# Performance work log

Hardware: AMD Instinct MI355X
Metric: run time of the kernel (lower is better)

The kernel has to match this reference:

```python
import jax, jax.numpy as jnp
import numpy as np

N = 50000      # nodes
DEG = 16       # in-degree per node -> E = 800k edges
IN = 256       # in_size
HID = 32       # hid_size
HEAD = 4       # heads in first layer
OUT = 40       # out_size (classes)
HH = HID * HEAD  # 128, hidden width
NEG_SLOPE = 0.2


def setup_inputs() -> dict:
    key = jax.random.key(0)
    ks = jax.random.split(key, 16)
    E = N * DEG
    src = jax.random.randint(ks[0], (E,), 0, N)
    dst = jnp.repeat(jnp.arange(N), DEG)  # every node has DEG in-edges

    def nrm(k, shape):
        return jax.random.normal(k, shape, jnp.float32) * 0.1

    return dict(
        features=jax.random.normal(ks[1], (N, IN), jnp.float32),
        src=src, dst=dst,
        # layer 1: GATConv(IN -> HID, HEAD heads)
        W1=nrm(ks[2], (IN, HH)), al1=nrm(ks[3], (HEAD, HID)), ar1=nrm(ks[4], (HEAD, HID)), b1=nrm(ks[5], (HH,)),
        # hidden layer: GATConv(HH -> HH, 1 head)
        Wh=nrm(ks[6], (HH, HH)), alh=nrm(ks[7], (1, HH)), arh=nrm(ks[8], (1, HH)), bh=nrm(ks[9], (HH,)),
        # layer 2: GATConv(HH -> OUT, 1 head)
        W2=nrm(ks[10], (HH, OUT)), al2=nrm(ks[11], (1, OUT)), ar2=nrm(ks[12], (1, OUT)), b2=nrm(ks[13], (OUT,)),
    )


def gat_conv(x, src, dst, W, al, ar, b):
    """DGL-style GATConv. x:[N,F], W:[F,H*D], al/ar:[H,D], b:[H*D]. Returns [N,H,D]."""
    n = x.shape[0]
    H, D = al.shape
    feat = (x @ W).reshape(n, H, D)                 # [N,H,D]
    el = jnp.sum(feat * al, axis=-1)                # [N,H]
    er = jnp.sum(feat * ar, axis=-1)                # [N,H]
    e = jax.nn.leaky_relu(el[src] + er[dst], NEG_SLOPE)  # [E,H] per-edge logits
    # segment softmax over each destination's in-edges
    emax = jax.lax.stop_gradient(jax.ops.segment_max(e, dst, num_segments=n))  # [N,H]
    ex = jnp.exp(e - emax[dst])                     # [E,H]
    den = jax.ops.segment_sum(ex, dst, num_segments=n)  # [N,H]
    alpha = ex / den[dst]                           # [E,H]
    out = jax.ops.segment_sum(feat[src] * alpha[:, :, None], dst, num_segments=n)  # [N,H,D]
    return out + b.reshape(1, H, D)


def reference(features, src, dst, W1, al1, ar1, b1, Wh, alh, arh, bh, W2, al2, ar2, b2):
    # conv1 -> flatten heads -> relu
    h = jax.nn.relu(gat_conv(features, src, dst, W1, al1, ar1, b1).reshape(N, HH))
    # hidden GATConv (1 head) -> mean over head -> relu (dropout is identity in eval)
    h = jax.nn.relu(gat_conv(h, src, dst, Wh, alh, arh, bh).mean(axis=1))
    # conv2 (1 head) -> mean over head -> log_softmax
    h = gat_conv(h, src, dst, W2, al2, ar2, b2).mean(axis=1)
    return jax.nn.log_softmax(h, axis=1)
```

## Files before the change

kernel.cpp:

```cpp
#include <hip/hip_runtime.h>
#include <cstddef>
#include <math.h>

#define NN 50000
#define DEG 16
#define NEG_SLOPE 0.2f

typedef __attribute__((ext_vector_type(8))) short bf16x8;
typedef __attribute__((ext_vector_type(4))) float f32x4;

__device__ inline unsigned short f2bf(float x) {
    unsigned u = __float_as_uint(x);
    return (unsigned short)((u + 0x7FFF + ((u >> 16) & 1)) >> 16);
}
__device__ inline float bf2f(unsigned short u) {
    return __uint_as_float(((unsigned)u) << 16);
}
__device__ inline unsigned pack_bf2(float lo, float hi) {
    return (unsigned)f2bf(lo) | ((unsigned)f2bf(hi) << 16);
}
__device__ inline void gld_lds16(const unsigned short* g, unsigned short* l) {
    __builtin_amdgcn_global_load_lds((const __attribute__((address_space(1))) void*)g,
                                     (__attribute__((address_space(3))) void*)l, 16, 0, 0);
}

__global__ void prep_k(const float* __restrict__ W1, unsigned short* __restrict__ Wt1,
                       const float* __restrict__ Wh, unsigned short* __restrict__ Wth,
                       const float* __restrict__ feats, unsigned short* __restrict__ fb)
{
    const int b = blockIdx.x;
    if (b < 128) {
        int idx = b * 256 + threadIdx.x;
        int c = idx >> 8, k = idx & 255;
        Wt1[idx] = f2bf(W1[(size_t)k * 128 + c]);
    } else if (b < 192) {
        int idx = (b - 128) * 256 + threadIdx.x;
        int c = idx >> 7, k = idx & 127;
        Wth[idx] = f2bf(Wh[(size_t)k * 128 + c]);
    } else {
        int i = (b - 192) * 256 + threadIdx.x;
        const float4* p = (const float4*)feats + (size_t)i * 2;
        float4 v0 = p[0], v1 = p[1];
        uint4 o;
        o.x = pack_bf2(v0.x, v0.y);
        o.y = pack_bf2(v0.z, v0.w);
        o.z = pack_bf2(v1.x, v1.y);
        o.w = pack_bf2(v1.z, v1.w);
        *(uint4*)&fb[(size_t)i * 8] = o;
    }
}

__launch_bounds__(256)
__global__ void gemm1_k(const unsigned short* __restrict__ A,
                        const unsigned short* __restrict__ Wt,
                        const float* __restrict__ al, const float* __restrict__ ar,
                        unsigned short* __restrict__ feat,
                        float* __restrict__ el, float* __restrict__ er)
{
    constexpr int K = 256, KS = K / 32, SLOTS = K * 2, PARTS = SLOTS / 256, TPB = 4;
    __shared__ __align__(16) unsigned short buf[2][SLOTS * 8];
    const int tid = threadIdx.x;
    const int w = tid >> 6, l = tid & 63;
    const int lr = l & 15, lq = l >> 4;
    const int col0 = w * 32;

    bf16x8 B0[KS], B1[KS];
#pragma unroll
    for (int ks = 0; ks < KS; ks++) {
        B0[ks] = *(const bf16x8*)(Wt + (size_t)(col0 + lr) * K + ks * 32 + lq * 8);
        B1[ks] = *(const bf16x8*)(Wt + (size_t)(col0 + 16 + lr) * K + ks * 32 + lq * 8);
    }

    const int t0 = blockIdx.x * TPB;
    const int tmax = NN / 16;
    const int t1 = (t0 + TPB < tmax) ? t0 + TPB : tmax;
    if (t0 >= tmax) return;

    auto stage = [&](int t, int b) {
#pragma unroll
        for (int p = 0; p < PARTS; p++) {
            int j = tid + p * 256;
            int row = t * 16 + (j & 15);
            int koff = (j >> 6) * 32 + ((j >> 4) & 3) * 8;
            gld_lds16(A + (size_t)row * K + koff, &buf[b][(size_t)j * 8]);
        }
    };
    stage(t0, t0 & 1);

    for (int t = t0; t < t1; ++t) {
        __syncthreads();
        if (t + 1 < t1) stage(t + 1, (t + 1) & 1);

        f32x4 acc0 = {0.f, 0.f, 0.f, 0.f}, acc1 = {0.f, 0.f, 0.f, 0.f};
        const unsigned short* bb = buf[t & 1];
#pragma unroll
        for (int ks = 0; ks < KS; ks++) {
            bf16x8 a = *(const bf16x8*)(bb + (size_t)(ks * 64 + l) * 8);
            acc0 = __builtin_amdgcn_mfma_f32_16x16x32_bf16(a, B0[ks], acc0, 0, 0, 0);
            acc1 = __builtin_amdgcn_mfma_f32_16x16x32_bf16(a, B1[ks], acc1, 0, 0, 0);
        }

        const int row0 = t * 16;
#pragma unroll
        for (int reg = 0; reg < 4; reg++) {
            const int r = row0 + lq * 4 + reg;
            feat[(size_t)r * 128 + col0 + lr]      = f2bf(acc0[reg]);
            feat[(size_t)r * 128 + col0 + 16 + lr] = f2bf(acc1[reg]);
        }

        float pe[4], pr[4];
#pragma unroll
        for (int reg = 0; reg < 4; reg++) {
            pe[reg] = acc0[reg] * al[col0 + lr] + acc1[reg] * al[col0 + 16 + lr];
            pr[reg] = acc0[reg] * ar[col0 + lr] + acc1[reg] * ar[col0 + 16 + lr];
        }
#pragma unroll
        for (int m = 1; m < 16; m <<= 1)
#pragma unroll
            for (int reg = 0; reg < 4; reg++) {
                pe[reg] += __shfl_xor(pe[reg], m);
                pr[reg] += __shfl_xor(pr[reg], m);
            }
        if (lr == 0) {
#pragma unroll
            for (int reg = 0; reg < 4; reg++) {
                const int r = row0 + lq * 4 + reg;
                el[r * 4 + w] = pe[reg];
                er[r * 4 + w] = pr[reg];
            }
        }
    }
}

__launch_bounds__(256)
__global__ void fusedh_k(const unsigned short* __restrict__ feat1,
                         const float* __restrict__ el1, const float* __restrict__ er1,
                         const int* __restrict__ src, const float* __restrict__ b1,
                         const unsigned short* __restrict__ Wt,
                         const float* __restrict__ alh, const float* __restrict__ arh,
                         unsigned short* __restrict__ feat2,
                         float* __restrict__ el, float* __restrict__ er)
{
    __shared__ __align__(16) unsigned short abuf[256 * 8];
    __shared__ float s_alpha[16][64];
    __shared__ float redE[4][16], redR[4][16];
    const int tid = threadIdx.x;
    const int w = tid >> 6, lane = tid & 63;
    const int q = lane >> 4, li = lane & 15;
    const int slot = w * 4 + q;
    const int row0 = blockIdx.x * 16;
    const int node = row0 + slot;
    const int col0 = w * 32;

    bf16x8 B0[4], B1[4];
#pragma unroll
    for (int ks = 0; ks < 4; ks++) {
        B0[ks] = *(const bf16x8*)(Wt + (size_t)(col0 + li) * 128 + ks * 32 + q * 8);
        B1[ks] = *(const bf16x8*)(Wt + (size_t)(col0 + 16 + li) * 128 + ks * 32 + q * 8);
    }

    const int s = src[node * DEG + li];
    {
        const float4 elv = *(const float4*)(el1 + (size_t)s * 4);
        const float4 erv = *(const float4*)(er1 + (size_t)node * 4);
        float e[4] = {elv.x + erv.x, elv.y + erv.y, elv.z + erv.z, elv.w + erv.w};
#pragma unroll
        for (int h = 0; h < 4; h++) {
            float x = e[h];
            x = (x > 0.f) ? x : NEG_SLOPE * x;
            float mx = x;
#pragma unroll
            for (int d = 1; d < 16; d <<= 1) mx = fmaxf(mx, __shfl_xor(mx, d, 16));
            float ex = expf(x - mx);
            float den = ex;
#pragma unroll
            for (int d = 1; d < 16; d <<= 1) den += __shfl_xor(den, d, 16);
            s_alpha[slot][h * 16 + li] = ex / den;
        }
    }
    uint4 v[16];
#pragma unroll
    for (int jj = 0; jj < 16; jj++) {
        int sj = __shfl(s, (lane & 48) | jj);
        v[jj] = *(const uint4*)(feat1 + (size_t)sj * 128 + li * 8);
    }
    float acc[8] = {0.f, 0.f, 0.f, 0.f, 0.f, 0.f, 0.f, 0.f};
    const int hrow = (li >> 2) * 16;
#pragma unroll
    for (int jj = 0; jj < 16; jj++) {
        float a = s_alpha[slot][hrow + jj];
        unsigned u0 = v[jj].x, u1 = v[jj].y, u2 = v[jj].z, u3 = v[jj].w;
        acc[0] += a * bf2f((unsigned short)(u0 & 0xFFFF));
        acc[1] += a * bf2f((unsigned short)(u0 >> 16));
        acc[2] += a * bf2f((unsigned short)(u1 & 0xFFFF));
        acc[3] += a * bf2f((unsigned short)(u1 >> 16));
        acc[4] += a * bf2f((unsigned short)(u2 & 0xFFFF));
        acc[5] += a * bf2f((unsigned short)(u2 >> 16));
        acc[6] += a * bf2f((unsigned short)(u3 & 0xFFFF));
        acc[7] += a * bf2f((unsigned short)(u3 >> 16));
    }
    const float4 bb0 = *(const float4*)(b1 + li * 8);
    const float4 bb1 = *(const float4*)(b1 + li * 8 + 4);
    float o[8];
    o[0] = fmaxf(acc[0] + bb0.x, 0.f); o[1] = fmaxf(acc[1] + bb0.y, 0.f);
    o[2] = fmaxf(acc[2] + bb0.z, 0.f); o[3] = fmaxf(acc[3] + bb0.w, 0.f);
    o[4] = fmaxf(acc[4] + bb1.x, 0.f); o[5] = fmaxf(acc[5] + bb1.y, 0.f);
    o[6] = fmaxf(acc[6] + bb1.z, 0.f); o[7] = fmaxf(acc[7] + bb1.w, 0.f);
    {
        uint4 pk;
        pk.x = pack_bf2(o[0], o[1]);
        pk.y = pack_bf2(o[2], o[3]);
        pk.z = pack_bf2(o[4], o[5]);
        pk.w = pack_bf2(o[6], o[7]);
        int jw = ((li >> 2) * 64 + (li & 3) * 16 + slot) ^ (li & 7);
        *(uint4*)&abuf[(size_t)jw * 8] = pk;
    }
    __syncthreads();

    f32x4 acc0 = {0.f, 0.f, 0.f, 0.f}, acc1 = {0.f, 0.f, 0.f, 0.f};
#pragma unroll
    for (int ks = 0; ks < 4; ks++) {
        int jr = (ks * 64 + lane) ^ ((ks * 4 + q) & 7);
        bf16x8 a = *(const bf16x8*)&abuf[(size_t)jr * 8];
        acc0 = __builtin_amdgcn_mfma_f32_16x16x32_bf16(a, B0[ks], acc0, 0, 0, 0);
        acc1 = __builtin_amdgcn_mfma_f32_16x16x32_bf16(a, B1[ks], acc1, 0, 0, 0);
    }

#pragma unroll
    for (int reg = 0; reg < 4; reg++) {
        const int r = row0 + q * 4 + reg;
        feat2[(size_t)r * 128 + col0 + li]      = f2bf(acc0[reg]);
        feat2[(size_t)r * 128 + col0 + 16 + li] = f2bf(acc1[reg]);
    }
    float pe[4], pr[4];
#pragma unroll
    for (int reg = 0; reg < 4; reg++) {
        pe[reg] = acc0[reg] * alh[col0 + li] + acc1[reg] * alh[col0 + 16 + li];
        pr[reg] = acc0[reg] * arh[col0 + li] + acc1[reg] * arh[col0 + 16 + li];
    }
#pragma unroll
    for (int m = 1; m < 16; m <<= 1)
#pragma unroll
        for (int reg = 0; reg < 4; reg++) {
            pe[reg] += __shfl_xor(pe[reg], m);
            pr[reg] += __shfl_xor(pr[reg], m);
        }
    if (li == 0) {
#pragma unroll
        for (int reg = 0; reg < 4; reg++) {
            redE[w][q * 4 + reg] = pe[reg];
            redR[w][q * 4 + reg] = pr[reg];
        }
    }
    __syncthreads();
    if (tid < 16) {
        el[row0 + tid] = redE[0][tid] + redE[1][tid] + redE[2][tid] + redE[3][tid];
        er[row0 + tid] = redR[0][tid] + redR[1][tid] + redR[2][tid] + redR[3][tid];
    }
}

__launch_bounds__(256)
__global__ void fused40_k(const unsigned short* __restrict__ feat2,
                          const float* __restrict__ elA, const float* __restrict__ erA,
                          const int* __restrict__ src, const float* __restrict__ bh,
                          const float* __restrict__ W2,
                          const float* __restrict__ al2, const float* __restrict__ ar2,
                          unsigned short* __restrict__ f40,
                          float* __restrict__ el2, float* __restrict__ er2)
{
    __shared__ float As[32][132];
    __shared__ float Ws[128 * 40];
    const int tid = threadIdx.x;
    const int w = tid >> 6, lane = tid & 63;
    const int q = lane >> 4, li = lane & 15;
    const int slot = w * 4 + q;
    const int row0 = blockIdx.x * 32;

    {
        const float4* s4 = (const float4*)W2;
        float4* d4 = (float4*)Ws;
#pragma unroll
        for (int p = 0; p < 5; p++) d4[tid + 256 * p] = s4[tid + 256 * p];
    }

#pragma unroll
    for (int rnd = 0; rnd < 2; rnd++) {
        const int row = rnd * 16 + slot;
        int node = row0 + row;
        if (node > NN - 1) node = NN - 1;
        const int s = src[node * DEG + li];
        float x = elA[s] + erA[node];
        x = (x > 0.f) ? x : NEG_SLOPE * x;
        float mx = x;
#pragma unroll
        for (int d = 1; d < 16; d <<= 1) mx = fmaxf(mx, __shfl_xor(mx, d, 16));
        float ex = expf(x - mx);
        float den = ex;
#pragma unroll
        for (int d = 1; d < 16; d <<= 1) den += __shfl_xor(den, d, 16);
        const float alpha = ex / den;

        uint4 v[16];
#pragma unroll
        for (int jj = 0; jj < 16; jj++) {
            int sj = __shfl(s, (lane & 48) | jj);
            v[jj] = *(const uint4*)(feat2 + (size_t)sj * 128 + li * 8);
        }
        float acc[8] = {0.f, 0.f, 0.f, 0.f, 0.f, 0.f, 0.f, 0.f};
#pragma unroll
        for (int jj = 0; jj < 16; jj++) {
            float a = __shfl(alpha, (lane & 48) | jj);
            unsigned u0 = v[jj].x, u1 = v[jj].y, u2 = v[jj].z, u3 = v[jj].w;
            acc[0] += a * bf2f((unsigned short)(u0 & 0xFFFF));
            acc[1] += a * bf2f((unsigned short)(u0 >> 16));
            acc[2] += a * bf2f((unsigned short)(u1 & 0xFFFF));
            acc[3] += a * bf2f((unsigned short)(u1 >> 16));
            acc[4] += a * bf2f((unsigned short)(u2 & 0xFFFF));
            acc[5] += a * bf2f((unsigned short)(u2 >> 16));
            acc[6] += a * bf2f((unsigned short)(u3 & 0xFFFF));
            acc[7] += a * bf2f((unsigned short)(u3 >> 16));
        }
        const float4 bb0 = *(const float4*)(bh + li * 8);
        const float4 bb1 = *(const float4*)(bh + li * 8 + 4);
        float4 o0, o1;
        o0.x = fmaxf(acc[0] + bb0.x, 0.f); o0.y = fmaxf(acc[1] + bb0.y, 0.f);
        o0.z = fmaxf(acc[2] + bb0.z, 0.f); o0.w = fmaxf(acc[3] + bb0.w, 0.f);
        o1.x = fmaxf(acc[4] + bb1.x, 0.f); o1.y = fmaxf(acc[5] + bb1.y, 0.f);
        o1.z = fmaxf(acc[6] + bb1.z, 0.f); o1.w = fmaxf(acc[7] + bb1.w, 0.f);
        *(float4*)&As[row][li * 8]     = o0;
        *(float4*)&As[row][li * 8 + 4] = o1;
    }
    __syncthreads();

    const int tx = tid & 31;
    const int ty = tid >> 5;
    const int ctx = (tx < 20) ? tx : 19;
    const float2* Wf2 = (const float2*)Ws;
    float acc[4][2] = {};
#pragma unroll 4
    for (int k = 0; k < 128; k++) {
        float2 wv = Wf2[k * 20 + ctx];
#pragma unroll
        for (int i = 0; i < 4; i++) {
            float a = As[ty * 4 + i][k];
            acc[i][0] += a * wv.x;
            acc[i][1] += a * wv.y;
        }
    }
    float pel[4], per[4];
#pragma unroll
    for (int i = 0; i < 4; i++) {
        float vl = 0.f, vr = 0.f;
        if (tx < 20) {
            vl = acc[i][0] * al2[2 * ctx] + acc[i][1] * al2[2 * ctx + 1];
            vr = acc[i][0] * ar2[2 * ctx] + acc[i][1] * ar2[2 * ctx + 1];
        }
        pel[i] = vl; per[i] = vr;
    }
#pragma unroll
    for (int m = 1; m < 32; m <<= 1) {
#pragma unroll
        for (int i = 0; i < 4; i++) {
            pel[i] += __shfl_xor(pel[i], m);
            per[i] += __shfl_xor(per[i], m);
        }
    }
#pragma unroll
    for (int i = 0; i < 4; i++) {
        int r = row0 + ty * 4 + i;
        if (r < NN) {
            if (tx < 20) *(unsigned*)&f40[(size_t)r * 40 + 2 * tx] = pack_bf2(acc[i][0], acc[i][1]);
            if (tx == 0) { el2[r] = pel[i]; er2[r] = per[i]; }
        }
    }
}

__launch_bounds__(256)
__global__ void agg40_ls_k(const unsigned short* __restrict__ feat, const float* __restrict__ el,
                           const float* __restrict__ er, const int* __restrict__ src,
                           const float* __restrict__ bias, float* __restrict__ out)
{
    __shared__ float s_alpha[8][DEG];
    __shared__ int s_src[8][DEG];
    const int tid = threadIdx.x;
    const int w = tid >> 6, lane = tid & 63;
    const int half = lane >> 5, li = lane & 31;
    const int slot = w * 2 + half;
    const int node = blockIdx.x * 8 + slot;
    const int j = li & 15;

    int s = src[node * DEG + j];
    float e = el[s] + er[node];
    e = (e > 0.f) ? e : NEG_SLOPE * e;
    float mx = e;
#pragma unroll
    for (int d = 1; d < 16; d <<= 1) mx = fmaxf(mx, __shfl_xor(mx, d));
    float ex = expf(e - mx);
    float den = ex;
#pragma unroll
    for (int d = 1; d < 16; d <<= 1) den += __shfl_xor(den, d);
    if (li < 16) { s_alpha[slot][j] = ex / den; s_src[slot][j] = s; }
    __syncthreads();

    float acc0 = 0.f, acc1 = 0.f;
    if (li < 20) {
#pragma unroll
        for (int jj = 0; jj < DEG; jj++) {
            int sj = s_src[slot][jj];
            float a = s_alpha[slot][jj];
            unsigned v = *(const unsigned*)(feat + (size_t)sj * 40 + 2 * li);
            acc0 += a * bf2f((unsigned short)(v & 0xFFFF));
            acc1 += a * bf2f((unsigned short)(v >> 16));
        }
    }
    float v0 = acc0 + bias[2 * li], v1 = acc1 + bias[2 * li + 1];
    float m2 = (li < 20) ? fmaxf(v0, v1) : -INFINITY;
#pragma unroll
    for (int d = 1; d < 32; d <<= 1) m2 = fmaxf(m2, __shfl_xor(m2, d));
    float pe = (li < 20) ? (expf(v0 - m2) + expf(v1 - m2)) : 0.f;
    float se = pe;
#pragma unroll
    for (int d = 1; d < 32; d <<= 1) se += __shfl_xor(se, d);
    if (li < 20) {
        float ls = m2 + logf(se);
        out[(size_t)node * 40 + 2 * li]     = v0 - ls;
        out[(size_t)node * 40 + 2 * li + 1] = v1 - ls;
    }
}

extern "C" void kernel_launch(void* const* d_in, const int* in_sizes, int n_in,
                              void* d_out, int out_size, void* d_ws, size_t ws_size,
                              hipStream_t stream)
{
    const float* features = (const float*)d_in[0];
    const int*   src      = (const int*)d_in[1];
    const float* W1  = (const float*)d_in[3];
    const float* al1 = (const float*)d_in[4];
    const float* ar1 = (const float*)d_in[5];
    const float* b1  = (const float*)d_in[6];
    const float* Wh  = (const float*)d_in[7];
    const float* alh = (const float*)d_in[8];
    const float* arh = (const float*)d_in[9];
    const float* bh  = (const float*)d_in[10];
    const float* W2  = (const float*)d_in[11];
    const float* al2 = (const float*)d_in[12];
    const float* ar2 = (const float*)d_in[13];
    const float* b2  = (const float*)d_in[14];
    float* out = (float*)d_out;

    float* ws = (float*)d_ws;
    unsigned short* featb  = (unsigned short*)ws;
    unsigned short* featb2 = featb + (size_t)NN * 128;
    float* el1  = (float*)(featb2 + (size_t)NN * 128);
    float* er1  = el1 + (size_t)NN * 4;
    float* elA  = er1 + (size_t)NN * 4;
    float* erA  = elA + NN;
    float* el2  = erA + NN;
    float* er2  = el2 + NN;
    unsigned short* f40b = (unsigned short*)(er2 + NN);
    unsigned short* Wt1  = f40b + (size_t)NN * 40;
    unsigned short* Wth  = Wt1 + 128 * 256;
    unsigned short* featbf = Wth + 128 * 128;

    dim3 blk(256);
    prep_k<<<6442, blk, 0, stream>>>(W1, Wt1, Wh, Wth, features, featbf);
    gemm1_k<<<782, blk, 0, stream>>>(featbf, Wt1, al1, ar1, featb, el1, er1);
    fusedh_k<<<3125, blk, 0, stream>>>(featb, el1, er1, src, b1, Wth, alh, arh,
                                       featb2, elA, erA);
    fused40_k<<<1563, blk, 0, stream>>>(featb2, elA, erA, src, bh, W2, al2, ar2,
                                        f40b, el2, er2);
    agg40_ls_k<<<6250, blk, 0, stream>>>(f40b, el2, er2, src, b2, out);
}
```

Before: 121.7 us.

## Fuse fp32-to-bf16 feature conversion into gemm1 and drop LDS staging in aggregation

The separate pass that converted the 50000x256 fp32 feature matrix to bf16 is removed. gemm1 now stages fp32 rows into LDS with an XOR swizzle and converts to bf16 just before the MFMA, which saves a full write and re-read of the converted features. Weight loads in fusedh and the W2 copy in fused40 are moved later, after the gather/softmax phase, to shorten register live ranges and overlap. agg40 replaces its shared-memory alpha/src staging and block barrier with warp shuffles. The trade-off is twice the LDS traffic and footprint in gemm1 plus per-element conversion ALU work inside the MFMA loop.

```diff
diff --git a/kernel.cpp b/kernel.cpp
--- a/kernel.cpp
+++ b/kernel.cpp
@@ -19,46 +19,35 @@
 __device__ inline unsigned pack_bf2(float lo, float hi) {
     return (unsigned)f2bf(lo) | ((unsigned)f2bf(hi) << 16);
 }
-__device__ inline void gld_lds16(const unsigned short* g, unsigned short* l) {
+__device__ inline void gld_lds16f(const float* g, float* l) {
     __builtin_amdgcn_global_load_lds((const __attribute__((address_space(1))) void*)g,
                                      (__attribute__((address_space(3))) void*)l, 16, 0, 0);
 }
 
 __global__ void prep_k(const float* __restrict__ W1, unsigned short* __restrict__ Wt1,
-                       const float* __restrict__ Wh, unsigned short* __restrict__ Wth,
-                       const float* __restrict__ feats, unsigned short* __restrict__ fb)
+                       const float* __restrict__ Wh, unsigned short* __restrict__ Wth)
 {
     const int b = blockIdx.x;
     if (b < 128) {
         int idx = b * 256 + threadIdx.x;
         int c = idx >> 8, k = idx & 255;
         Wt1[idx] = f2bf(W1[(size_t)k * 128 + c]);
-    } else if (b < 192) {
+    } else {
         int idx = (b - 128) * 256 + threadIdx.x;
         int c = idx >> 7, k = idx & 127;
         Wth[idx] = f2bf(Wh[(size_t)k * 128 + c]);
-    } else {
-        int i = (b - 192) * 256 + threadIdx.x;
-        const float4* p = (const float4*)feats + (size_t)i * 2;
-        float4 v0 = p[0], v1 = p[1];
-        uint4 o;
-        o.x = pack_bf2(v0.x, v0.y);
-        o.y = pack_bf2(v0.z, v0.w);
-        o.z = pack_bf2(v1.x, v1.y);
-        o.w = pack_bf2(v1.z, v1.w);
-        *(uint4*)&fb[(size_t)i * 8] = o;
     }
 }
 
 __launch_bounds__(256)
-__global__ void gemm1_k(const unsigned short* __restrict__ A,
+__global__ void gemm1_k(const float* __restrict__ A,
                         const unsigned short* __restrict__ Wt,
                         const float* __restrict__ al, const float* __restrict__ ar,
                         unsigned short* __restrict__ feat,
                         float* __restrict__ el, float* __restrict__ er)
 {
-    constexpr int K = 256, KS = K / 32, SLOTS = K * 2, PARTS = SLOTS / 256, TPB = 4;
-    __shared__ __align__(16) unsigned short buf[2][SLOTS * 8];
+    constexpr int K = 256, KS = 8, TPB = 4;
+    __shared__ __align__(16) float buf[2][4096];
     const int tid = threadIdx.x;
     const int w = tid >> 6, l = tid & 63;
     const int lr = l & 15, lq = l >> 4;
@@ -78,11 +67,11 @@
 
     auto stage = [&](int t, int b) {
 #pragma unroll
-        for (int p = 0; p < PARTS; p++) {
+        for (int p = 0; p < 4; p++) {
             int j = tid + p * 256;
-            int row = t * 16 + (j & 15);
-            int koff = (j >> 6) * 32 + ((j >> 4) & 3) * 8;
-            gld_lds16(A + (size_t)row * K + koff, &buf[b][(size_t)j * 8]);
+            int row = j >> 6;
+            int kg = (j & 63) ^ (row & 7);
+            gld_lds16f(A + (size_t)(t * 16 + row) * 256 + kg * 4, &buf[b][(size_t)j * 4]);
         }
     };
     stage(t0, t0 & 1);
@@ -92,10 +81,18 @@
         if (t + 1 < t1) stage(t + 1, (t + 1) & 1);
 
         f32x4 acc0 = {0.f, 0.f, 0.f, 0.f}, acc1 = {0.f, 0.f, 0.f, 0.f};
-        const unsigned short* bb = buf[t & 1];
+        const float* bb = buf[t & 1];
 #pragma unroll
         for (int ks = 0; ks < KS; ks++) {
-            bf16x8 a = *(const bf16x8*)(bb + (size_t)(ks * 64 + l) * 8);
+            const int kg0 = ks * 8 + lq * 2;
+            const int s0 = lr * 64 + (kg0 ^ (lr & 7));
+            const int s1 = lr * 64 + ((kg0 + 1) ^ (lr & 7));
+            float4 va = *(const float4*)&bb[(size_t)s0 * 4];
+            float4 vb = *(const float4*)&bb[(size_t)s1 * 4];
+            bf16x8 a = {(short)f2bf(va.x), (short)f2bf(va.y),
+                        (short)f2bf(va.z), (short)f2bf(va.w),
+                        (short)f2bf(vb.x), (short)f2bf(vb.y),
+                        (short)f2bf(vb.z), (short)f2bf(vb.w)};
             acc0 = __builtin_amdgcn_mfma_f32_16x16x32_bf16(a, B0[ks], acc0, 0, 0, 0);
             acc1 = __builtin_amdgcn_mfma_f32_16x16x32_bf16(a, B1[ks], acc1, 0, 0, 0);
         }
@@ -151,13 +148,6 @@
     const int row0 = blockIdx.x * 16;
     const int node = row0 + slot;
     const int col0 = w * 32;
-
-    bf16x8 B0[4], B1[4];
-#pragma unroll
-    for (int ks = 0; ks < 4; ks++) {
-        B0[ks] = *(const bf16x8*)(Wt + (size_t)(col0 + li) * 128 + ks * 32 + q * 8);
-        B1[ks] = *(const bf16x8*)(Wt + (size_t)(col0 + 16 + li) * 128 + ks * 32 + q * 8);
-    }
 
     const int s = src[node * DEG + li];
     {
@@ -215,6 +205,13 @@
         int jw = ((li >> 2) * 64 + (li & 3) * 16 + slot) ^ (li & 7);
         *(uint4*)&abuf[(size_t)jw * 8] = pk;
     }
+
+    bf16x8 B0[4], B1[4];
+#pragma unroll
+    for (int ks = 0; ks < 4; ks++) {
+        B0[ks] = *(const bf16x8*)(Wt + (size_t)(col0 + li) * 128 + ks * 32 + q * 8);
+        B1[ks] = *(const bf16x8*)(Wt + (size_t)(col0 + 16 + li) * 128 + ks * 32 + q * 8);
+    }
     __syncthreads();
 
     f32x4 acc0 = {0.f, 0.f, 0.f, 0.f}, acc1 = {0.f, 0.f, 0.f, 0.f};
@@ -275,13 +272,6 @@
     const int q = lane >> 4, li = lane & 15;
     const int slot = w * 4 + q;
     const int row0 = blockIdx.x * 32;
-
-    {
-        const float4* s4 = (const float4*)W2;
-        float4* d4 = (float4*)Ws;
-#pragma unroll
-        for (int p = 0; p < 5; p++) d4[tid + 256 * p] = s4[tid + 256 * p];
-    }
 
 #pragma unroll
     for (int rnd = 0; rnd < 2; rnd++) {
@@ -330,6 +320,12 @@
         *(float4*)&As[row][li * 8]     = o0;
         *(float4*)&As[row][li * 8 + 4] = o1;
     }
+    {
+        const float4* s4 = (const float4*)W2;
+        float4* d4 = (float4*)Ws;
+#pragma unroll
+        for (int p = 0; p < 5; p++) d4[tid + 256 * p] = s4[tid + 256 * p];
+    }
     __syncthreads();
 
     const int tx = tid & 31;
@@ -380,47 +376,41 @@
                            const float* __restrict__ er, const int* __restrict__ src,
                            const float* __restrict__ bias, float* __restrict__ out)
 {
-    __shared__ float s_alpha[8][DEG];
-    __shared__ int s_src[8][DEG];
     const int tid = threadIdx.x;
     const int w = tid >> 6, lane = tid & 63;
     const int half = lane >> 5, li = lane & 31;
-    const int slot = w * 2 + half;
-    const int node = blockIdx.x * 8 + slot;
-    const int j = li & 15;
-
-    int s = src[node * DEG + j];
+    const int node = blockIdx.x * 8 + w * 2 + half;
+
+    const int s = src[node * DEG + (li & 15)];
     float e = el[s] + er[node];
     e = (e > 0.f) ? e : NEG_SLOPE * e;
     float mx = e;
 #pragma unroll
-    for (int d = 1; d < 16; d <<= 1) mx = fmaxf(mx, __shfl_xor(mx, d));
+    for (int d = 1; d < 16; d <<= 1) mx = fmaxf(mx, __shfl_xor(mx, d, 16));
     float ex = expf(e - mx);
     float den = ex;
 #pragma unroll
-    for (int d = 1; d < 16; d <<= 1) den += __shfl_xor(den, d);
-    if (li < 16) { s_alpha[slot][j] = ex / den; s_src[slot][j] = s; }
-    __syncthreads();
-
+    for (int d = 1; d < 16; d <<= 1) den += __shfl_xor(den, d, 16);
+    const float alpha = ex / den;
+
+    const int cli = (li < 20) ? li : 19;
     float acc0 = 0.f, acc1 = 0.f;
-    if (li < 20) {
-#pragma unroll
-        for (int jj = 0; jj < DEG; jj++) {
-            int sj = s_src[slot][jj];
-            float a = s_alpha[slot][jj];
-            unsigned v = *(const unsigned*)(feat + (size_t)sj * 40 + 2 * li);
-            acc0 += a * bf2f((unsigned short)(v & 0xFFFF));
-            acc1 += a * bf2f((unsigned short)(v >> 16));
-        }
-    }
-    float v0 = acc0 + bias[2 * li], v1 = acc1 + bias[2 * li + 1];
+#pragma unroll
+    for (int jj = 0; jj < DEG; jj++) {
+        int sj = __shfl(s, jj, 32);
+        float a = __shfl(alpha, jj, 32);
+        unsigned v = *(const unsigned*)(feat + (size_t)sj * 40 + 2 * cli);
+        acc0 += a * bf2f((unsigned short)(v & 0xFFFF));
+        acc1 += a * bf2f((unsigned short)(v >> 16));
+    }
+    float v0 = acc0 + bias[2 * cli], v1 = acc1 + bias[2 * cli + 1];
     float m2 = (li < 20) ? fmaxf(v0, v1) : -INFINITY;
 #pragma unroll
-    for (int d = 1; d < 32; d <<= 1) m2 = fmaxf(m2, __shfl_xor(m2, d));
+    for (int d = 1; d < 32; d <<= 1) m2 = fmaxf(m2, __shfl_xor(m2, d, 32));
     float pe = (li < 20) ? (expf(v0 - m2) + expf(v1 - m2)) : 0.f;
     float se = pe;
 #pragma unroll
-    for (int d = 1; d < 32; d <<= 1) se += __shfl_xor(se, d);
+    for (int d = 1; d < 32; d <<= 1) se += __shfl_xor(se, d, 32);
     if (li < 20) {
         float ls = m2 + logf(se);
         out[(size_t)node * 40 + 2 * li]     = v0 - ls;
@@ -460,11 +450,10 @@
     unsigned short* f40b = (unsigned short*)(er2 + NN);
     unsigned short* Wt1  = f40b + (size_t)NN * 40;
     unsigned short* Wth  = Wt1 + 128 * 256;
-    unsigned short* featbf = Wth + 128 * 128;
 
     dim3 blk(256);
-    prep_k<<<6442, blk, 0, stream>>>(W1, Wt1, Wh, Wth, features, featbf);
-    gemm1_k<<<782, blk, 0, stream>>>(featbf, Wt1, al1, ar1, featb, el1, er1);
+    prep_k<<<192, blk, 0, stream>>>(W1, Wt1, Wh, Wth);
+    gemm1_k<<<782, blk, 0, stream>>>(features, Wt1, al1, ar1, featb, el1, er1);
     fusedh_k<<<3125, blk, 0, stream>>>(featb, el1, er1, src, b1, Wth, alh, arh,
                                        featb2, elA, erA);
     fused40_k<<<1563, blk, 0, stream>>>(featb2, elA, erA, src, bh, W2, al2, ar2,
```

Result: no change. 119.9 us (-1.5%).
